# Performance work log

Hardware: AMD Instinct MI355X
Metric: run time of the kernel (lower is better)

Reference implementation:

```python
import jax, jax.numpy as jnp
import numpy as np

DIMENSIONS = 1000
NUM_LEVELS = 10
SIZE = 28
BATCH = 256
NUM_CLASSES = 10


def setup_inputs() -> dict:
    key = jax.random.key(0)
    k1, k2, k3 = jax.random.split(key, 3)
    # pixel values in [0, 1]
    x = jax.random.uniform(k1, (BATCH, SIZE, SIZE), dtype=jnp.float32)
    # fixed bipolar position hypervectors (bundle of x/y Level HVs); use +-1 like MAP HVs
    position = jnp.where(jax.random.normal(k2, (SIZE * SIZE, DIMENSIONS)) > 0, 1.0, -1.0).astype(jnp.float32)
    # Level value embedding table
    value_table = jnp.where(jax.random.normal(k3, (NUM_LEVELS, DIMENSIONS)) > 0, 1.0, -1.0).astype(jnp.float32)
    # classifier weight, initialized to zero in the original module
    W = jnp.zeros((NUM_CLASSES, DIMENSIONS), dtype=jnp.float32)
    return {"x": x, "position": position, "value_table": value_table, "W": W}


def reference(x, position, value_table, W):
    B = x.shape[0]
    xf = x.reshape(B, -1)  # [B, P] flatten
    # torchhd Level value_to_index with low=0, high=1
    idx = jnp.clip(jnp.round(xf * (NUM_LEVELS - 1)), 0, NUM_LEVELS - 1).astype(jnp.int32)
    hv = value_table[idx]                         # gather: [B, P, D]
    bound = position[None, :, :] * hv             # bind:   [B, P, D]
    s = jnp.sum(bound, axis=1)                    # multiset sum over pixels: [B, D]
    enc = jnp.where(s > 0, 1.0, -1.0).astype(x.dtype)  # hard_quantize
    logit = enc @ W.T                             # [B, num_classes]
    return logit
```

## Files before the change

### kernel.cpp

```cpp
#include <hip/hip_runtime.h>
#include <stdint.h>

#define DIMS   1000
#define NLEV   10
#define NPIX   784
#define NBATCH 256
#define NCLS   10
#define WPD    32

__global__ __launch_bounds__(256) void pack_ballot(const float* __restrict__ position,
                                                   const float* __restrict__ value_table,
                                                   uint64_t* __restrict__ ws64) {
    const int t    = threadIdx.x;
    const int lane = t & 63;
    const int wv   = (blockIdx.x * 256 + t) >> 6;
    const int nw   = (gridDim.x * 256) >> 6;
    for (int r = wv; r < NPIX + NLEV; r += nw) {
        const float* src = (r < NPIX) ? (position + (size_t)r * DIMS)
                                      : (value_table + (size_t)(r - NPIX) * DIMS);
        #pragma unroll
        for (int k = 0; k < 16; ++k) {
            int d = k * 64 + lane;
            float v = (d < DIMS) ? src[d] : 0.f;
            uint64_t m = __ballot(v > 0.f);
            if (lane == 0) ws64[(size_t)r * 16 + k] = m;
        }
    }
}

__device__ __forceinline__ void fa(uint32_t a, uint32_t b, uint32_t cin,
                                   uint32_t& s, uint32_t& c) {
    uint32_t t = a ^ b;
    s = t ^ cin;
    c = (a & b) | (t & cin);
}

__global__ __launch_bounds__(512) void hdc_main(const float* __restrict__ x,
                                                const float* __restrict__ W,
                                                const uint32_t* __restrict__ ws_bits,
                                                float* __restrict__ out) {
    __shared__ uint32_t s_idx[NPIX];
    __shared__ uint32_t s_vt[NLEV * WPD];
    __shared__ uint32_t s_cnt1[32 * 8 * 7];
    __shared__ uint32_t s_cnt2[32 * 4 * 8];
    __shared__ uint32_t s_cnt3[32 * 2 * 9];
    __shared__ uint32_t s_cnt4_enc[32];
    __shared__ float    s_red[8][NCLS];

    const int b = blockIdx.x;
    const int t = threadIdx.x;

    for (int p = t; p < NPIX; p += 512) {
        float v = x[b * NPIX + p] * 9.0f;
        int l = (int)rintf(v);
        l = l < 0 ? 0 : (l > 9 ? 9 : l);
        s_idx[p] = (uint32_t)(l * WPD);
    }
    if (t < NLEV * WPD) s_vt[t] = ws_bits[NPIX * WPD + t];
    __syncthreads();

    const int w = t & 31;
    const int g = t >> 5;

    uint32_t p0 = 0, p1 = 0, p2 = 0, p3 = 0, p4 = 0, p5 = 0;

    for (int c = 0; c < 6; ++c) {
        uint32_t idxv[8], posv[8], xv[8];
        #pragma unroll
        for (int j = 0; j < 8; ++j)
            idxv[j] = s_idx[g + 128 * c + 16 * j];
        #pragma unroll
        for (int j = 0; j < 8; ++j)
            posv[j] = ws_bits[(g + 128 * c + 16 * j) * WPD + w];
        #pragma unroll
        for (int j = 0; j < 8; ++j)
            xv[j] = posv[j] ^ s_vt[idxv[j] + w];
        uint32_t sa, ca, sb, cb, sc, cc, sd, cd, se, ce, sf, cf, cg;
        fa(xv[0], xv[1], xv[2], sa, ca);
        fa(xv[3], xv[4], xv[5], sb, cb);
        fa(xv[6], xv[7], p0,   sc, cc);
        fa(sa, sb, sc, p0, cd);
        fa(ca, cb, cc, se, ce);
        fa(se, cd, p1, p1, cf);
        fa(ce, cf, p2, p2, cg);
        uint32_t tmp = p3 & cg; p3 ^= cg;
        uint32_t tm2 = p4 & tmp; p4 ^= tmp;
        p5 ^= tm2;
    }
    {
        uint32_t xb = ws_bits[(g + 768) * WPD + w] ^ s_vt[s_idx[g + 768] + w];
        uint32_t c = xb, tmp;
        tmp = p0 & c; p0 ^= c; c = tmp;
        tmp = p1 & c; p1 ^= c; c = tmp;
        tmp = p2 & c; p2 ^= c; c = tmp;
        tmp = p3 & c; p3 ^= c; c = tmp;
        tmp = p4 & c; p4 ^= c; c = tmp;
        p5 ^= c;
    }

    {
        uint32_t q0 = __shfl_down(p0, 32), q1 = __shfl_down(p1, 32),
                 q2 = __shfl_down(p2, 32), q3 = __shfl_down(p3, 32),
                 q4 = __shfl_down(p4, 32), q5 = __shfl_down(p5, 32);
        uint32_t r0, r1, r2, r3, r4, r5, r6, c, tt;
        c  = p0 & q0; r0 = p0 ^ q0;
        tt = p1 ^ q1; r1 = tt ^ c; c = (p1 & q1) | (tt & c);
        tt = p2 ^ q2; r2 = tt ^ c; c = (p2 & q2) | (tt & c);
        tt = p3 ^ q3; r3 = tt ^ c; c = (p3 & q3) | (tt & c);
        tt = p4 ^ q4; r4 = tt ^ c; c = (p4 & q4) | (tt & c);
        tt = p5 ^ q5; r5 = tt ^ c; c = (p5 & q5) | (tt & c);
        r6 = c;
        const int wid = t >> 6;
        if ((t & 63) < 32) {
            int base = (w * 8 + wid) * 7;
            s_cnt1[base + 0] = r0; s_cnt1[base + 1] = r1; s_cnt1[base + 2] = r2;
            s_cnt1[base + 3] = r3; s_cnt1[base + 4] = r4; s_cnt1[base + 5] = r5;
            s_cnt1[base + 6] = r6;
        }
    }
    __syncthreads();

    if (t < 128) {
        int w2 = t & 31, j = t >> 5;
        int ba = (w2 * 8 + 2 * j) * 7, bb = (w2 * 8 + 2 * j + 1) * 7;
        uint32_t c = 0, tt;
        int bo = (w2 * 4 + j) * 8;
        #pragma unroll
        for (int i = 0; i < 7; ++i) {
            uint32_t a = s_cnt1[ba + i], bv = s_cnt1[bb + i];
            tt = a ^ bv; s_cnt2[bo + i] = tt ^ c; c = (a & bv) | (tt & c);
        }
        s_cnt2[bo + 7] = c;
    }
    __syncthreads();

    if (t < 64) {
        int w2 = t & 31, j = t >> 5;
        int ba = (w2 * 4 + 2 * j) * 8, bb = (w2 * 4 + 2 * j + 1) * 8;
        uint32_t c = 0, tt;
        int bo = (w2 * 2 + j) * 9;
        #pragma unroll
        for (int i = 0; i < 8; ++i) {
            uint32_t a = s_cnt2[ba + i], bv = s_cnt2[bb + i];
            tt = a ^ bv; s_cnt3[bo + i] = tt ^ c; c = (a & bv) | (tt & c);
        }
        s_cnt3[bo + 8] = c;
    }
    __syncthreads();

    if (t < 32) {
        int ba = (t * 2) * 9, bb = (t * 2 + 1) * 9;
        uint32_t cnt[10];
        uint32_t c = 0, tt;
        #pragma unroll
        for (int i = 0; i < 9; ++i) {
            uint32_t a = s_cnt3[ba + i], bv = s_cnt3[bb + i];
            tt = a ^ bv; cnt[i] = tt ^ c; c = (a & bv) | (tt & c);
        }
        cnt[9] = c;
        uint32_t cy = 0;
        cy = cnt[3];
        cy = cnt[4] | cy;
        cy = cnt[5] | cy;
        cy = cnt[6] | cy;
        cy = cnt[7] & cy;
        cy = cnt[8] & cy;
        cy = cnt[9] | cy;
        s_cnt4_enc[t] = ~cy;
    }
    __syncthreads();

    float partial[NCLS];
    #pragma unroll
    for (int cc = 0; cc < NCLS; ++cc) partial[cc] = 0.f;

    if (t < 500) {
        int d0 = 2 * t;
        uint32_t ew = s_cnt4_enc[d0 >> 5];
        float e0 = ((ew >> (d0 & 31)) & 1u) ? 1.0f : -1.0f;
        float e1 = ((ew >> ((d0 + 1) & 31)) & 1u) ? 1.0f : -1.0f;
        #pragma unroll
        for (int cc = 0; cc < NCLS; ++cc) {
            const float2* wv = (const float2*)(W + cc * DIMS + d0);
            float2 wl = *wv;
            partial[cc] = e0 * wl.x + e1 * wl.y;
        }
    }
    #pragma unroll
    for (int cc = 0; cc < NCLS; ++cc) {
        #pragma unroll
        for (int off = 32; off > 0; off >>= 1)
            partial[cc] += __shfl_down(partial[cc], off);
    }
    const int lane = t & 63, wid = t >> 6;
    if (lane == 0) {
        #pragma unroll
        for (int cc = 0; cc < NCLS; ++cc) s_red[wid][cc] = partial[cc];
    }
    __syncthreads();
    if (t < NCLS) {
        float acc = 0.f;
        #pragma unroll
        for (int v = 0; v < 8; ++v) acc += s_red[v][t];
        out[b * NCLS + t] = acc;
    }
}

extern "C" void kernel_launch(void* const* d_in, const int* in_sizes, int n_in,
                              void* d_out, int out_size, void* d_ws, size_t ws_size,
                              hipStream_t stream) {
    const float* x        = (const float*)d_in[0];
    const float* position = (const float*)d_in[1];
    const float* vtab     = (const float*)d_in[2];
    const float* W        = (const float*)d_in[3];
    float* out            = (float*)d_out;

    pack_ballot<<<200, 256, 0, stream>>>(position, vtab, (uint64_t*)d_ws);
    hdc_main<<<NBATCH, 512, 0, stream>>>(x, W, (const uint32_t*)d_ws, out);
}
```

Measured before the change: 72.35 us.

## Prefetch W and position bits early, collapse count reduction into one stage

```diff
diff --git a/kernel.cpp b/kernel.cpp
--- a/kernel.cpp
+++ b/kernel.cpp
@@ -41,14 +41,21 @@
                                                 float* __restrict__ out) {
     __shared__ uint32_t s_idx[NPIX];
     __shared__ uint32_t s_vt[NLEV * WPD];
-    __shared__ uint32_t s_cnt1[32 * 8 * 7];
-    __shared__ uint32_t s_cnt2[32 * 4 * 8];
-    __shared__ uint32_t s_cnt3[32 * 2 * 9];
-    __shared__ uint32_t s_cnt4_enc[32];
+    __shared__ uint32_t s_cnt1[7 * 256];
+    __shared__ uint32_t s_enc[32];
     __shared__ float    s_red[8][NCLS];
 
-    const int b = blockIdx.x;
-    const int t = threadIdx.x;
+    const int b    = blockIdx.x;
+    const int t    = threadIdx.x;
+    const int lane = t & 63;
+    const int wid  = t >> 6;
+
+    float2 wreg[NCLS];
+    if (t < 500) {
+        #pragma unroll
+        for (int cc = 0; cc < NCLS; ++cc)
+            wreg[cc] = *(const float2*)(W + cc * DIMS + 2 * t);
+    }
 
     for (int p = t; p < NPIX; p += 512) {
         float v = x[b * NPIX + p] * 9.0f;
@@ -64,26 +71,33 @@
 
     uint32_t p0 = 0, p1 = 0, p2 = 0, p3 = 0, p4 = 0, p5 = 0;
 
+    uint32_t posn[8];
+    #pragma unroll
+    for (int j = 0; j < 8; ++j)
+        posn[j] = ws_bits[(g + 16 * j) * WPD + w];
+
     for (int c = 0; c < 6; ++c) {
-        uint32_t idxv[8], posv[8], xv[8];
+        uint32_t posv[8];
+        #pragma unroll
+        for (int j = 0; j < 8; ++j) posv[j] = posn[j];
+        if (c < 5) {
+            #pragma unroll
+            for (int j = 0; j < 8; ++j)
+                posn[j] = ws_bits[(g + 128 * (c + 1) + 16 * j) * WPD + w];
+        }
+        uint32_t xv[8];
         #pragma unroll
         for (int j = 0; j < 8; ++j)
-            idxv[j] = s_idx[g + 128 * c + 16 * j];
-        #pragma unroll
-        for (int j = 0; j < 8; ++j)
-            posv[j] = ws_bits[(g + 128 * c + 16 * j) * WPD + w];
-        #pragma unroll
-        for (int j = 0; j < 8; ++j)
-            xv[j] = posv[j] ^ s_vt[idxv[j] + w];
-        uint32_t sa, ca, sb, cb, sc, cc, sd, cd, se, ce, sf, cf, cg;
+            xv[j] = posv[j] ^ s_vt[s_idx[g + 128 * c + 16 * j] + w];
+        uint32_t sa, ca, sb, cb, sc, cc, cd, se, ce, cf, cg2;
         fa(xv[0], xv[1], xv[2], sa, ca);
         fa(xv[3], xv[4], xv[5], sb, cb);
         fa(xv[6], xv[7], p0,   sc, cc);
         fa(sa, sb, sc, p0, cd);
         fa(ca, cb, cc, se, ce);
         fa(se, cd, p1, p1, cf);
-        fa(ce, cf, p2, p2, cg);
-        uint32_t tmp = p3 & cg; p3 ^= cg;
+        fa(ce, cf, p2, p2, cg2);
+        uint32_t tmp = p3 & cg2; p3 ^= cg2;
         uint32_t tm2 = p4 & tmp; p4 ^= tmp;
         p5 ^= tm2;
     }
@@ -110,63 +124,46 @@
         tt = p4 ^ q4; r4 = tt ^ c; c = (p4 & q4) | (tt & c);
         tt = p5 ^ q5; r5 = tt ^ c; c = (p5 & q5) | (tt & c);
         r6 = c;
-        const int wid = t >> 6;
         if ((t & 63) < 32) {
-            int base = (w * 8 + wid) * 7;
-            s_cnt1[base + 0] = r0; s_cnt1[base + 1] = r1; s_cnt1[base + 2] = r2;
-            s_cnt1[base + 3] = r3; s_cnt1[base + 4] = r4; s_cnt1[base + 5] = r5;
-            s_cnt1[base + 6] = r6;
-        }
-    }
-    __syncthreads();
-
-    if (t < 128) {
-        int w2 = t & 31, j = t >> 5;
-        int ba = (w2 * 8 + 2 * j) * 7, bb = (w2 * 8 + 2 * j + 1) * 7;
-        uint32_t c = 0, tt;
-        int bo = (w2 * 4 + j) * 8;
-        #pragma unroll
-        for (int i = 0; i < 7; ++i) {
-            uint32_t a = s_cnt1[ba + i], bv = s_cnt1[bb + i];
-            tt = a ^ bv; s_cnt2[bo + i] = tt ^ c; c = (a & bv) | (tt & c);
-        }
-        s_cnt2[bo + 7] = c;
-    }
-    __syncthreads();
-
-    if (t < 64) {
-        int w2 = t & 31, j = t >> 5;
-        int ba = (w2 * 4 + 2 * j) * 8, bb = (w2 * 4 + 2 * j + 1) * 8;
-        uint32_t c = 0, tt;
-        int bo = (w2 * 2 + j) * 9;
-        #pragma unroll
-        for (int i = 0; i < 8; ++i) {
-            uint32_t a = s_cnt2[ba + i], bv = s_cnt2[bb + i];
-            tt = a ^ bv; s_cnt3[bo + i] = tt ^ c; c = (a & bv) | (tt & c);
-        }
-        s_cnt3[bo + 8] = c;
+            int base = wid * 32 + w;
+            s_cnt1[0 * 256 + base] = r0; s_cnt1[1 * 256 + base] = r1;
+            s_cnt1[2 * 256 + base] = r2; s_cnt1[3 * 256 + base] = r3;
+            s_cnt1[4 * 256 + base] = r4; s_cnt1[5 * 256 + base] = r5;
+            s_cnt1[6 * 256 + base] = r6;
+        }
     }
     __syncthreads();
 
     if (t < 32) {
-        int ba = (t * 2) * 9, bb = (t * 2 + 1) * 9;
-        uint32_t cnt[10];
-        uint32_t c = 0, tt;
-        #pragma unroll
-        for (int i = 0; i < 9; ++i) {
-            uint32_t a = s_cnt3[ba + i], bv = s_cnt3[bb + i];
-            tt = a ^ bv; cnt[i] = tt ^ c; c = (a & bv) | (tt & c);
-        }
-        cnt[9] = c;
-        uint32_t cy = 0;
-        cy = cnt[3];
-        cy = cnt[4] | cy;
-        cy = cnt[5] | cy;
-        cy = cnt[6] | cy;
-        cy = cnt[7] & cy;
-        cy = cnt[8] & cy;
-        cy = cnt[9] | cy;
-        s_cnt4_enc[t] = ~cy;
+        uint32_t acc[10];
+        #pragma unroll
+        for (int i = 0; i < 7; ++i) acc[i] = s_cnt1[i * 256 + t];
+        acc[7] = acc[8] = acc[9] = 0u;
+        #pragma unroll
+        for (int gg = 1; gg < 8; ++gg) {
+            uint32_t c = 0, tt;
+            #pragma unroll
+            for (int i = 0; i < 7; ++i) {
+                uint32_t a = acc[i], bv = s_cnt1[i * 256 + gg * 32 + t];
+                tt = a ^ bv;
+                acc[i] = tt ^ c;
+                c = (a & bv) | (tt & c);
+            }
+            #pragma unroll
+            for (int i = 7; i < 10; ++i) {
+                uint32_t a = acc[i];
+                acc[i] = a ^ c;
+                c = a & c;
+            }
+        }
+        uint32_t cy = acc[3];
+        cy = acc[4] | cy;
+        cy = acc[5] | cy;
+        cy = acc[6] | cy;
+        cy = acc[7] & cy;
+        cy = acc[8] & cy;
+        cy = acc[9] | cy;
+        s_enc[t] = ~cy;
     }
     __syncthreads();
 
@@ -176,15 +173,12 @@
 
     if (t < 500) {
         int d0 = 2 * t;
-        uint32_t ew = s_cnt4_enc[d0 >> 5];
+        uint32_t ew = s_enc[d0 >> 5];
         float e0 = ((ew >> (d0 & 31)) & 1u) ? 1.0f : -1.0f;
         float e1 = ((ew >> ((d0 + 1) & 31)) & 1u) ? 1.0f : -1.0f;
         #pragma unroll
-        for (int cc = 0; cc < NCLS; ++cc) {
-            const float2* wv = (const float2*)(W + cc * DIMS + d0);
-            float2 wl = *wv;
-            partial[cc] = e0 * wl.x + e1 * wl.y;
-        }
+        for (int cc = 0; cc < NCLS; ++cc)
+            partial[cc] = e0 * wreg[cc].x + e1 * wreg[cc].y;
     }
     #pragma unroll
     for (int cc = 0; cc < NCLS; ++cc) {
@@ -192,7 +186,6 @@
         for (int off = 32; off > 0; off >>= 1)
             partial[cc] += __shfl_down(partial[cc], off);
     }
-    const int lane = t & 63, wid = t >> 6;
     if (lane == 0) {
         #pragma unroll
         for (int cc = 0; cc < NCLS; ++cc) s_red[wid][cc] = partial[cc];
```

After: 73.24 us. No clear change (+1.2%).
